# Kernel tuning notes

Measured on AMD Instinct MI355X. Metric: run time of the kernel, lower is better.

## Reference

```python
import math
import jax, jax.numpy as jnp
import numpy as np

NUM_HEADS = 16
EMBED = 1024
B, T = 2, 2048


def setup_inputs() -> dict:
    key = jax.random.key(0)
    k1, k2 = jax.random.split(key)
    x = jax.random.normal(k1, (B, T, EMBED), dtype=jnp.float32)
    # kaiming-uniform-style init for [num_heads*embed, embed]
    bound = 1.0 / math.sqrt(NUM_HEADS * EMBED)
    weight = jax.random.uniform(k2, (NUM_HEADS * EMBED, EMBED), dtype=jnp.float32,
                                minval=-bound, maxval=bound)
    return {"x": x, "weight": weight}


def reference(x, weight):
    b, t, c = x.shape
    nh = NUM_HEADS
    hs = c // nh
    # b t (nh hs) -> b nh t hs
    y = x.reshape(b, t, nh, hs).transpose(0, 2, 1, 3)
    # scores: [b, nh, t, t], scaled by sqrt(hs) (yt.shape[-2] == hs)
    scores = jnp.einsum('bhtk,bhsk->bhts', y, y) / math.sqrt(hs)
    attn = jax.nn.softmax(scores, axis=-1)
    # value is raw x broadcast per head; contract without materializing the repeat
    o = jnp.einsum('bhts,bsc->bhtc', attn, x)          # [b, nh, t, c]
    o = o.transpose(0, 2, 1, 3).reshape(b, t, nh * c)  # b nh t c -> b t (nh c)
    return o @ weight                                   # [b, t, c]
```

## Files before the change

### kernel.cpp

```cpp
#include <hip/hip_runtime.h>
#include <hip/hip_bf16.h>


typedef __hip_bfloat16 bf16;
typedef __bf16 bf16x8 __attribute__((ext_vector_type(8)));
typedef float f32x4 __attribute__((ext_vector_type(4)));

#define B_ 2
#define T_ 2048
#define C_ 1024
#define H_ 16
#define D_ 16384
#define E_ 1024
#define KZ_ 4

__device__ __forceinline__ void load_lds16(const void* g, void* l) {
  __builtin_amdgcn_global_load_lds(
      (const __attribute__((address_space(1))) void*)g,
      (__attribute__((address_space(3))) void*)l, 16, 0, 0);
}

__device__ __forceinline__ unsigned pack2(float a, float b) {
  union { bf16 h[2]; unsigned u; } p;
  p.h[0] = __float2bfloat16(a);
  p.h[1] = __float2bfloat16(b);
  return p.u;
}

__global__ __launch_bounds__(256) void transpose_cast_kernel(
    const float* __restrict__ in, bf16* __restrict__ out, int rows, int cols) {
  __shared__ float tile[32][33];
  size_t zoff = (size_t)blockIdx.z * rows * cols;
  int c0 = blockIdx.x * 32, r0 = blockIdx.y * 32;
  int tx = threadIdx.x, ty = threadIdx.y;
  for (int i = ty; i < 32; i += 8)
    tile[i][tx] = in[zoff + (size_t)(r0 + i) * cols + c0 + tx];
  __syncthreads();
  for (int i = ty; i < 32; i += 8)
    out[zoff + (size_t)(c0 + i) * rows + r0 + tx] = __float2bfloat16(tile[tx][i]);
}

__global__ __launch_bounds__(256) void xh_cast_kernel(
    const float* __restrict__ x, bf16* __restrict__ xh) {
  int bt = blockIdx.x;
  int b = bt >> 11, t = bt & (T_ - 1);
  float4 v = ((const float4*)(x + (size_t)bt * C_))[threadIdx.x];
  int c = threadIdx.x * 4;
  int h = c >> 6, k = c & 63;
  bf16* o = xh + ((size_t)(b * H_ + h) * T_ + t) * 64 + k;
  o[0] = __float2bfloat16(v.x);
  o[1] = __float2bfloat16(v.y);
  o[2] = __float2bfloat16(v.z);
  o[3] = __float2bfloat16(v.w);
}

__global__ __launch_bounds__(256) void reduce_kernel(
    const float* __restrict__ p, float* __restrict__ out, int n4) {
  int i = blockIdx.x * 256 + threadIdx.x;
  if (i >= n4) return;
  float4 a = ((const float4*)p)[i];
#pragma unroll
  for (int z = 1; z < KZ_; ++z) {
    float4 b = ((const float4*)(p + (size_t)z * n4 * 4))[i];
    a.x += b.x; a.y += b.y; a.z += b.z; a.w += b.w;
  }
  ((float4*)out)[i] = a;
}

__global__ __launch_bounds__(256) void scores_kernel(
    const bf16* __restrict__ xh,
    bf16* __restrict__ P,
    float* __restrict__ lsum) {
  int L = blockIdx.x;
  int z = blockIdx.y;
  int ti = 0, rem = L;
  while (rem >= H_ - ti) { rem -= H_ - ti; ++ti; }
  int tj = ti + rem;

  const bf16* A = xh + (size_t)z * T_ * 64;
  bf16* Pz = P + (size_t)z * T_ * T_;
  size_t row0 = (size_t)ti * 128, col0 = (size_t)tj * 128;

  __shared__ bf16 lds_a[128 * 64];
  __shared__ bf16 lds_b[128 * 64];
  int t = threadIdx.x;

  const bf16* ga = A + (row0 + (t >> 3)) * 64 + (t & 7) * 8;
  const bf16* gb = A + (col0 + (t >> 3)) * 64 + (t & 7) * 8;
#pragma unroll
  for (int q = 0; q < 4; ++q) {
    load_lds16(ga + q * 32 * 64, lds_a + t * 8 + q * 2048);
    load_lds16(gb + q * 32 * 64, lds_b + t * 8 + q * 2048);
  }
  __syncthreads();

  int lane = t & 63, w = t >> 6;
  int wm = (w & 1) * 64, wn = (w >> 1) * 64;
  int lr = lane & 15, lq = lane >> 4;
  const int a_off = (wm + lr) * 64 + lq * 8;
  const int b_off = (wn + lr) * 64 + lq * 8;

  f32x4 acc[4][4] = {};
#pragma unroll
  for (int kh = 0; kh < 2; ++kh) {
    bf16x8 af[4], bfr[4];
#pragma unroll
    for (int i = 0; i < 4; ++i)
      af[i] = *(const bf16x8*)&lds_a[a_off + kh * 32 + i * 16 * 64];
#pragma unroll
    for (int j = 0; j < 4; ++j)
      bfr[j] = *(const bf16x8*)&lds_b[b_off + kh * 32 + j * 16 * 64];
#pragma unroll
    for (int i = 0; i < 4; ++i)
#pragma unroll
      for (int j = 0; j < 4; ++j)
        acc[i][j] = __builtin_amdgcn_mfma_f32_16x16x32_bf16(af[i], bfr[j],
                                                            acc[i][j], 0, 0, 0);
  }

  float rs[4][4];
  float cs[4];
#pragma unroll
  for (int i2 = 0; i2 < 4; ++i2)
#pragma unroll
    for (int reg = 0; reg < 4; ++reg) rs[i2][reg] = 0.f;
#pragma unroll
  for (int j2 = 0; j2 < 4; ++j2) cs[j2] = 0.f;

#pragma unroll
  for (int i2 = 0; i2 < 4; ++i2) {
    size_t rb = row0 + wm + i2 * 16 + lq * 4;
#pragma unroll
    for (int j2 = 0; j2 < 4; ++j2) {
      size_t c = col0 + wn + j2 * 16 + lr;
      float e[4];
#pragma unroll
      for (int reg = 0; reg < 4; ++reg) {
        e[reg] = __expf(acc[i2][j2][reg] * 0.125f);
        rs[i2][reg] += e[reg];
        cs[j2] += e[reg];
        Pz[(rb + reg) * T_ + c] = __float2bfloat16(e[reg]);
      }
      uint2 mv;
      mv.x = pack2(e[0], e[1]);
      mv.y = pack2(e[2], e[3]);
      *(uint2*)&Pz[c * T_ + rb] = mv;
    }
  }

#pragma unroll
  for (int i2 = 0; i2 < 4; ++i2)
#pragma unroll
    for (int reg = 0; reg < 4; ++reg) {
#pragma unroll
      for (int off = 1; off < 16; off <<= 1)
        rs[i2][reg] += __shfl_xor(rs[i2][reg], off);
    }
  if (lr == 0) {
#pragma unroll
    for (int i2 = 0; i2 < 4; ++i2) {
      size_t rb = row0 + wm + i2 * 16 + lq * 4;
#pragma unroll
      for (int reg = 0; reg < 4; ++reg)
        atomicAdd(&lsum[(size_t)z * T_ + rb + reg], rs[i2][reg]);
    }
  }
  if (ti != tj) {
#pragma unroll
    for (int j2 = 0; j2 < 4; ++j2) {
      cs[j2] += __shfl_xor(cs[j2], 16);
      cs[j2] += __shfl_xor(cs[j2], 32);
    }
    if (lq == 0) {
#pragma unroll
      for (int j2 = 0; j2 < 4; ++j2) {
        size_t c = col0 + wn + j2 * 16 + lr;
        atomicAdd(&lsum[(size_t)z * T_ + c], cs[j2]);
      }
    }
  }
}

template <int MODE, int SWZ>
__global__ __launch_bounds__(256) void gemm_bt_kernel(
    const bf16* __restrict__ A, long long a_zstride, int lda,
    const bf16* __restrict__ BT, long long b_zstride, int ldb,
    void* __restrict__ Cout, int ldc, long long c_zflat,
    const float* __restrict__ lsum, int lzs, int K) {
  __shared__ bf16 lds_a[128 * 64];
  __shared__ bf16 lds_b[128 * 64];
  int t = threadIdx.x;

  int bx = blockIdx.x, by = blockIdx.y, bz = blockIdx.z;
  if (SWZ) {
    int gx = gridDim.x, gy = gridDim.y, gz = gridDim.z;
    int S = gy * gz, nb = gx * S;
    if (((S & 7) == 0) && ((nb & 7) == 0)) {
      int L = bx + gx * (by + gy * bz);
      int xcd = L & 7, m = L >> 3, spx = S >> 3;
      int col = m % gx, sl = m / gx;
      int strip = xcd * spx + sl;
      bx = col; by = strip % gy; bz = strip / gy;
    }
  }

  const bf16* Ab = A + (size_t)bz * a_zstride;
  const bf16* Bb = BT + (size_t)bz * b_zstride;
  size_t row0 = (size_t)by * 128;
  size_t col0 = (size_t)bx * 128;

  const bf16* ga = Ab + (row0 + (t >> 3)) * (size_t)lda + (t & 7) * 8;
  const bf16* gb = Bb + (col0 + (t >> 3)) * (size_t)ldb + (t & 7) * 8;
  bf16* la = lds_a + t * 8;
  bf16* lb = lds_b + t * 8;

  f32x4 acc[4][4] = {};
  int lane = t & 63;
  int w = t >> 6;
  int wm = (w & 1) * 64, wn = (w >> 1) * 64;
  int lr = lane & 15, lq = lane >> 4;
  const int a_off = (wm + lr) * 64 + lq * 8;
  const int b_off = (wn + lr) * 64 + lq * 8;

  for (int k0 = 0; k0 < K; k0 += 64) {
#pragma unroll
    for (int q = 0; q < 4; ++q) {
      load_lds16(ga + (size_t)q * 32 * lda, la + q * 2048);
      load_lds16(gb + (size_t)q * 32 * ldb, lb + q * 2048);
    }
    ga += 64;
    gb += 64;
    __syncthreads();

#pragma unroll
    for (int kh = 0; kh < 2; ++kh) {
      bf16x8 af[4], bfr[4];
#pragma unroll
      for (int i = 0; i < 4; ++i)
        af[i] = *(const bf16x8*)&lds_a[a_off + kh * 32 + i * 16 * 64];
#pragma unroll
      for (int j = 0; j < 4; ++j)
        bfr[j] = *(const bf16x8*)&lds_b[b_off + kh * 32 + j * 16 * 64];
#pragma unroll
      for (int i = 0; i < 4; ++i)
#pragma unroll
        for (int j = 0; j < 4; ++j)
          acc[i][j] = __builtin_amdgcn_mfma_f32_16x16x32_bf16(
              af[i], bfr[j], acc[i][j], 0, 0, 0);
    }
    __syncthreads();
  }

  size_t cbase = (size_t)bz * c_zflat + col0;
#pragma unroll
  for (int i = 0; i < 4; ++i) {
    size_t r = row0 + wm + i * 16 + lq * 4;
    float4 inv4 = make_float4(1.f, 1.f, 1.f, 1.f);
    if (MODE == 3) {
      float4 lv = *(const float4*)&lsum[(size_t)bz * lzs + r];
      inv4 = make_float4(1.f / lv.x, 1.f / lv.y, 1.f / lv.z, 1.f / lv.w);
    }
#pragma unroll
    for (int j = 0; j < 4; ++j) {
      size_t c = cbase + wn + j * 16 + lr;
#pragma unroll
      for (int reg = 0; reg < 4; ++reg) {
        float v = acc[i][j][reg];
        size_t idx = (r + reg) * (size_t)ldc + c;
        if (MODE == 0) {
          ((float*)Cout)[idx] = v;
        } else {
          float iv = reg == 0 ? inv4.x : reg == 1 ? inv4.y : reg == 2 ? inv4.z
                                                                      : inv4.w;
          ((bf16*)Cout)[idx] = __float2bfloat16(v * iv);
        }
      }
    }
  }
}

extern "C" void kernel_launch(void* const* d_in, const int* in_sizes, int n_in,
                              void* d_out, int out_size, void* d_ws,
                              size_t ws_size, hipStream_t stream) {
  const float* x = (const float*)d_in[0];
  const float* wgt = (const float*)d_in[1];
  float* out = (float*)d_out;

  bf16* xbT = (bf16*)d_ws;
  bf16* wbT = xbT + (size_t)B_ * C_ * T_;
  bf16* xh = wbT + (size_t)E_ * D_;
  bf16* Obuf = xh + (size_t)B_ * H_ * T_ * 64;
  float* lsum = (float*)(Obuf + (size_t)B_ * T_ * D_);
  bf16* P = (bf16*)(lsum + (size_t)16 * T_);
  float* partials = (float*)P;

  transpose_cast_kernel<<<dim3(C_ / 32, T_ / 32, B_), dim3(32, 8), 0, stream>>>(
      x, xbT, T_, C_);
  transpose_cast_kernel<<<dim3(E_ / 32, D_ / 32, 1), dim3(32, 8), 0, stream>>>(
      wgt, wbT, D_, E_);
  xh_cast_kernel<<<B_ * T_, 256, 0, stream>>>(x, xh);

  size_t fixed_bytes = ((size_t)B_ * C_ * T_ + (size_t)E_ * D_ +
                        (size_t)B_ * H_ * T_ * 64 + (size_t)B_ * T_ * D_) * 2 +
                       (size_t)16 * T_ * 4;
  int Hs = 16;
  while (Hs > 1 && fixed_bytes + (size_t)Hs * T_ * T_ * 2 > ws_size) Hs >>= 1;
  int ntri = Hs == 16 ? 136 : 136;
  (void)ntri;

  for (int b = 0; b < B_; ++b) {
    for (int h0 = 0; h0 < H_; h0 += Hs) {
      const bf16* xhb = xh + (size_t)(b * H_ + h0) * T_ * 64;
      hipMemsetAsync(lsum, 0, (size_t)Hs * T_ * sizeof(float), stream);
      scores_kernel<<<dim3(136, Hs), 256, 0, stream>>>(xhb, P, lsum);
      gemm_bt_kernel<3, 1><<<dim3(C_ / 128, T_ / 128, Hs), 256, 0, stream>>>(
          P, (long long)T_ * T_, T_, xbT + (size_t)b * C_ * T_, 0LL, T_,
          (void*)(Obuf + (size_t)b * T_ * D_ + (size_t)h0 * C_), D_,
          (long long)C_, lsum, T_, T_);
    }
  }
  gemm_bt_kernel<0, 1><<<dim3(E_ / 128, (B_ * T_) / 128, KZ_), 256, 0,
                         stream>>>(Obuf, (long long)(D_ / KZ_), D_, wbT,
                                   (long long)(D_ / KZ_), D_, (void*)partials,
                                   E_, (long long)B_ * T_ * E_, nullptr, 0,
                                   D_ / KZ_);
  reduce_kernel<<<(B_ * T_ * E_ / 4 + 255) / 256, 256, 0, stream>>>(
      partials, out, B_ * T_ * E_ / 4);
}
```

Baseline: 898.0 us.

## Shrink GEMM K-tile, pack bf16 stores, bf16 split-K partials with more splits

The GEMM K-step drops from 64 to 32, which halves LDS use per block, and the launch bounds now ask for 4 blocks per CU to raise occupancy. Row-major stores in the scores and GEMM epilogues are paired through a lane shuffle into 32-bit packed bf16 writes. The final projection uses 8 split-K slices instead of 4, stores its partials as bf16 rather than fp32, and the reduce kernel sums 8 bf16 values per thread. Storing partials in bf16 adds rounding error before the sum, and the shorter K-step means twice as many barriers per unit of work.

```diff
diff --git a/kernel.cpp b/kernel.cpp
--- a/kernel.cpp
+++ b/kernel.cpp
@@ -12,7 +12,7 @@
 #define H_ 16
 #define D_ 16384
 #define E_ 1024
-#define KZ_ 4
+#define KZ_ 8
 
 __device__ __forceinline__ void load_lds16(const void* g, void* l) {
   __builtin_amdgcn_global_load_lds(
@@ -55,16 +55,20 @@
 }
 
 __global__ __launch_bounds__(256) void reduce_kernel(
-    const float* __restrict__ p, float* __restrict__ out, int n4) {
+    const bf16* __restrict__ p, float* __restrict__ out, int n8) {
   int i = blockIdx.x * 256 + threadIdx.x;
-  if (i >= n4) return;
-  float4 a = ((const float4*)p)[i];
-#pragma unroll
-  for (int z = 1; z < KZ_; ++z) {
-    float4 b = ((const float4*)(p + (size_t)z * n4 * 4))[i];
-    a.x += b.x; a.y += b.y; a.z += b.z; a.w += b.w;
-  }
-  ((float4*)out)[i] = a;
+  if (i >= n8) return;
+  float a[8] = {};
+#pragma unroll
+  for (int z = 0; z < KZ_; ++z) {
+    bf16x8 v = ((const bf16x8*)(p + (size_t)z * n8 * 8))[i];
+#pragma unroll
+    for (int k = 0; k < 8; ++k) a[k] += (float)v[k];
+  }
+  float4 lo = make_float4(a[0], a[1], a[2], a[3]);
+  float4 hi = make_float4(a[4], a[5], a[6], a[7]);
+  ((float4*)out)[2 * i] = lo;
+  ((float4*)out)[2 * i + 1] = hi;
 }
 
 __global__ __launch_bounds__(256) void scores_kernel(
@@ -139,7 +143,9 @@
         e[reg] = __expf(acc[i2][j2][reg] * 0.125f);
         rs[i2][reg] += e[reg];
         cs[j2] += e[reg];
-        Pz[(rb + reg) * T_ + c] = __float2bfloat16(e[reg]);
+        float nb = __shfl_xor(e[reg], 1);
+        if ((lr & 1) == 0)
+          *(unsigned*)&Pz[(rb + reg) * T_ + c] = pack2(e[reg], nb);
       }
       uint2 mv;
       mv.x = pack2(e[0], e[1]);
@@ -182,13 +188,13 @@
 }
 
 template <int MODE, int SWZ>
-__global__ __launch_bounds__(256) void gemm_bt_kernel(
+__global__ __launch_bounds__(256, 4) void gemm_bt_kernel(
     const bf16* __restrict__ A, long long a_zstride, int lda,
     const bf16* __restrict__ BT, long long b_zstride, int ldb,
     void* __restrict__ Cout, int ldc, long long c_zflat,
     const float* __restrict__ lsum, int lzs, int K) {
-  __shared__ bf16 lds_a[128 * 64];
-  __shared__ bf16 lds_b[128 * 64];
+  __shared__ bf16 lds_a[128 * 32];
+  __shared__ bf16 lds_b[128 * 32];
   int t = threadIdx.x;
 
   int bx = blockIdx.x, by = blockIdx.y, bz = blockIdx.z;
@@ -209,8 +215,8 @@
   size_t row0 = (size_t)by * 128;
   size_t col0 = (size_t)bx * 128;
 
-  const bf16* ga = Ab + (row0 + (t >> 3)) * (size_t)lda + (t & 7) * 8;
-  const bf16* gb = Bb + (col0 + (t >> 3)) * (size_t)ldb + (t & 7) * 8;
+  const bf16* ga = Ab + (row0 + (t >> 2)) * (size_t)lda + (t & 3) * 8;
+  const bf16* gb = Bb + (col0 + (t >> 2)) * (size_t)ldb + (t & 3) * 8;
   bf16* la = lds_a + t * 8;
   bf16* lb = lds_b + t * 8;
 
@@ -219,35 +225,31 @@
   int w = t >> 6;
   int wm = (w & 1) * 64, wn = (w >> 1) * 64;
   int lr = lane & 15, lq = lane >> 4;
-  const int a_off = (wm + lr) * 64 + lq * 8;
-  const int b_off = (wn + lr) * 64 + lq * 8;
-
-  for (int k0 = 0; k0 < K; k0 += 64) {
-#pragma unroll
-    for (int q = 0; q < 4; ++q) {
-      load_lds16(ga + (size_t)q * 32 * lda, la + q * 2048);
-      load_lds16(gb + (size_t)q * 32 * ldb, lb + q * 2048);
-    }
-    ga += 64;
-    gb += 64;
+  const int a_off0 = (wm + lr) * 32 + lq * 8;
+  const int b_off0 = (wn + lr) * 32 + lq * 8;
+
+  for (int k0 = 0; k0 < K; k0 += 32) {
+    load_lds16(ga, la);
+    load_lds16(ga + 64 * (size_t)lda, la + 64 * 32);
+    load_lds16(gb, lb);
+    load_lds16(gb + 64 * (size_t)ldb, lb + 64 * 32);
+    ga += 32;
+    gb += 32;
     __syncthreads();
 
-#pragma unroll
-    for (int kh = 0; kh < 2; ++kh) {
-      bf16x8 af[4], bfr[4];
-#pragma unroll
-      for (int i = 0; i < 4; ++i)
-        af[i] = *(const bf16x8*)&lds_a[a_off + kh * 32 + i * 16 * 64];
+    bf16x8 af[4], bfr[4];
+#pragma unroll
+    for (int i = 0; i < 4; ++i)
+      af[i] = *(const bf16x8*)&lds_a[a_off0 + i * 16 * 32];
+#pragma unroll
+    for (int j = 0; j < 4; ++j)
+      bfr[j] = *(const bf16x8*)&lds_b[b_off0 + j * 16 * 32];
+#pragma unroll
+    for (int i = 0; i < 4; ++i)
 #pragma unroll
       for (int j = 0; j < 4; ++j)
-        bfr[j] = *(const bf16x8*)&lds_b[b_off + kh * 32 + j * 16 * 64];
-#pragma unroll
-      for (int i = 0; i < 4; ++i)
-#pragma unroll
-        for (int j = 0; j < 4; ++j)
-          acc[i][j] = __builtin_amdgcn_mfma_f32_16x16x32_bf16(
-              af[i], bfr[j], acc[i][j], 0, 0, 0);
-    }
+        acc[i][j] = __builtin_amdgcn_mfma_f32_16x16x32_bf16(af[i], bfr[j],
+                                                            acc[i][j], 0, 0, 0);
     __syncthreads();
   }
 
@@ -266,13 +268,15 @@
 #pragma unroll
       for (int reg = 0; reg < 4; ++reg) {
         float v = acc[i][j][reg];
-        size_t idx = (r + reg) * (size_t)ldc + c;
-        if (MODE == 0) {
-          ((float*)Cout)[idx] = v;
-        } else {
+        if (MODE == 3) {
           float iv = reg == 0 ? inv4.x : reg == 1 ? inv4.y : reg == 2 ? inv4.z
                                                                       : inv4.w;
-          ((bf16*)Cout)[idx] = __float2bfloat16(v * iv);
+          v *= iv;
+        }
+        float nb = __shfl_xor(v, 1);
+        if ((lr & 1) == 0) {
+          size_t idx = (r + reg) * (size_t)ldc + c;
+          *(unsigned*)&((bf16*)Cout)[idx] = pack2(v, nb);
         }
       }
     }
@@ -292,7 +296,7 @@
   bf16* Obuf = xh + (size_t)B_ * H_ * T_ * 64;
   float* lsum = (float*)(Obuf + (size_t)B_ * T_ * D_);
   bf16* P = (bf16*)(lsum + (size_t)16 * T_);
-  float* partials = (float*)P;
+  bf16* partials = P;
 
   transpose_cast_kernel<<<dim3(C_ / 32, T_ / 32, B_), dim3(32, 8), 0, stream>>>(
       x, xbT, T_, C_);
@@ -305,8 +309,6 @@
                        (size_t)16 * T_ * 4;
   int Hs = 16;
   while (Hs > 1 && fixed_bytes + (size_t)Hs * T_ * T_ * 2 > ws_size) Hs >>= 1;
-  int ntri = Hs == 16 ? 136 : 136;
-  (void)ntri;
 
   for (int b = 0; b < B_; ++b) {
     for (int h0 = 0; h0 < H_; h0 += Hs) {
@@ -319,11 +321,11 @@
           (long long)C_, lsum, T_, T_);
     }
   }
-  gemm_bt_kernel<0, 1><<<dim3(E_ / 128, (B_ * T_) / 128, KZ_), 256, 0,
+  gemm_bt_kernel<1, 1><<<dim3(E_ / 128, (B_ * T_) / 128, KZ_), 256, 0,
                          stream>>>(Obuf, (long long)(D_ / KZ_), D_, wbT,
                                    (long long)(D_ / KZ_), D_, (void*)partials,
                                    E_, (long long)B_ * T_ * E_, nullptr, 0,
                                    D_ / KZ_);
-  reduce_kernel<<<(B_ * T_ * E_ / 4 + 255) / 256, 256, 0, stream>>>(
-      partials, out, B_ * T_ * E_ / 4);
-}
+  reduce_kernel<<<(B_ * T_ * E_ / 8 + 255) / 256, 256, 0, stream>>>(
+      partials, out, B_ * T_ * E_ / 8);
+}
```

After: 755.6 us. 15.9% less time.
